# Optimization experiments

Measured on AMD Instinct MI355X. Metric: run time of the kernel, lower is better.

The kernel has to match this reference:

```python
import jax, jax.numpy as jnp
import numpy as np

B, S, D = 4, 2048, 1024


def setup_inputs() -> dict:
    key = jax.random.key(0)
    k1, k2, k3, k4 = jax.random.split(key, 4)
    scale = 1.0 / np.sqrt(D)
    return {
        "X_emb": jax.random.normal(k1, (B, S, D), dtype=jnp.float32),
        "W_q": jax.random.normal(k2, (D, D), dtype=jnp.float32) * scale,
        "W_k": jax.random.normal(k3, (D, D), dtype=jnp.float32) * scale,
        "W_v": jax.random.normal(k4, (D, D), dtype=jnp.float32) * scale,
    }


def reference(X_emb, W_q, W_k, W_v):
    # nn.Linear(bias=False): x @ W.T
    Xq = jnp.einsum('bsd,ed->bse', X_emb, W_q)
    Xk = jnp.einsum('bsd,ed->bse', X_emb, W_k)
    Xv = jnp.einsum('bsd,ed->bse', X_emb, W_v)
    S_len = X_emb.shape[-2]
    # scores [B, S, S]; causal mask (strict upper triangle -> -inf)
    att = jnp.einsum('bqe,bke->bqk', Xq, Xk)
    causal = jnp.tril(jnp.ones((S_len, S_len), dtype=bool))
    att = jnp.where(causal, att, -jnp.inf)
    # note: original masks before scaling; -inf / sqrt(d) is still -inf
    att = att / jnp.sqrt(jnp.asarray(Xk.shape[-1], att.dtype))
    w = jax.nn.softmax(att, axis=-1)
    return jnp.einsum('bqk,bke->bqe', w, Xv)
```

## Files before the change

### kernel.cpp

```cpp
#include <hip/hip_runtime.h>
#include <stdint.h>
#include <math.h>

typedef __attribute__((ext_vector_type(8))) __bf16 bf16x8;
typedef __attribute__((ext_vector_type(4))) float f32x4;

__device__ __forceinline__ unsigned short f2bf(float f) {
    unsigned u = __float_as_uint(f);
    u += 0x7FFF + ((u >> 16) & 1);
    return (unsigned short)(u >> 16);
}
__device__ __forceinline__ float bf2f(unsigned short u) {
    return __uint_as_float((unsigned)u << 16);
}

__global__ __launch_bounds__(256)
void convt_k(const float* __restrict__ X, const float* __restrict__ Wq,
             const float* __restrict__ Wk, const float* __restrict__ Wv,
             unsigned short* __restrict__ Xb, unsigned short* __restrict__ XbT,
             unsigned short* __restrict__ WqT, unsigned short* __restrict__ WkT,
             unsigned short* __restrict__ Wvb) {
    const int S = 2048, D = 1024;
    const int z = blockIdx.z;
    const float* src;
    unsigned short* dstP = nullptr;
    unsigned short* dstT = nullptr;
    int rows;
    if (z < 4)      { src = X + (size_t)z * S * D; dstP = Xb + (size_t)z * S * D;
                      dstT = XbT + (size_t)z * D * S; rows = S; }
    else if (z == 4){ src = Wq; dstT = WqT; rows = D; }
    else if (z == 5){ src = Wk; dstT = WkT; rows = D; }
    else            { src = Wv; dstP = Wvb; rows = D; }
    const int r0 = blockIdx.y * 64, c0 = blockIdx.x * 64;
    if (r0 >= rows) return;

    __shared__ float tile[64][65];
    const int t = threadIdx.x;
    const int tr = t >> 4;
    const int tc4 = t & 15;
#pragma unroll
    for (int p = 0; p < 4; ++p) {
        int r = p * 16 + tr;
        float4 v = *reinterpret_cast<const float4*>(&src[(size_t)(r0 + r) * 1024 + c0 + tc4 * 4]);
        if (dstP) {
            ushort4 o; o.x = f2bf(v.x); o.y = f2bf(v.y); o.z = f2bf(v.z); o.w = f2bf(v.w);
            *reinterpret_cast<ushort4*>(&dstP[(size_t)(r0 + r) * 1024 + c0 + tc4 * 4]) = o;
        }
        if (dstT) {
            tile[r][tc4 * 4 + 0] = v.x; tile[r][tc4 * 4 + 1] = v.y;
            tile[r][tc4 * 4 + 2] = v.z; tile[r][tc4 * 4 + 3] = v.w;
        }
    }
    if (!dstT) return;
    __syncthreads();
    const int ldT = rows;
#pragma unroll
    for (int p = 0; p < 4; ++p) {
        int c = p * 16 + tr;
        ushort4 o;
        o.x = f2bf(tile[tc4 * 4 + 0][c]);
        o.y = f2bf(tile[tc4 * 4 + 1][c]);
        o.z = f2bf(tile[tc4 * 4 + 2][c]);
        o.w = f2bf(tile[tc4 * 4 + 3][c]);
        *reinterpret_cast<ushort4*>(&dstT[(size_t)(c0 + c) * ldT + r0 + tc4 * 4]) = o;
    }
}

__global__ __launch_bounds__(256)
void reduce4_k(const float* __restrict__ p, unsigned short* __restrict__ o, int n4) {
    const int slab = 1024 * 1024 / 4;
    int i = blockIdx.x * blockDim.x + threadIdx.x;
    int stride = gridDim.x * blockDim.x;
    for (; i < n4; i += stride) {
        float4 a = reinterpret_cast<const float4*>(p)[i];
        float4 b = reinterpret_cast<const float4*>(p)[i + slab];
        float4 c = reinterpret_cast<const float4*>(p)[i + 2 * slab];
        float4 d = reinterpret_cast<const float4*>(p)[i + 3 * slab];
        ushort4 u;
        u.x = f2bf(a.x + b.x + c.x + d.x);
        u.y = f2bf(a.y + b.y + c.y + d.y);
        u.z = f2bf(a.z + b.z + c.z + d.z);
        u.w = f2bf(a.w + b.w + c.w + d.w);
        reinterpret_cast<ushort4*>(o)[i] = u;
    }
}

__device__ __forceinline__ void gload16(const unsigned short* g, unsigned short* l) {
    __builtin_amdgcn_global_load_lds(
        (const __attribute__((address_space(1))) unsigned int*)g,
        (__attribute__((address_space(3))) unsigned int*)l, 16, 0, 0);
}

template <typename CT, int MODE>
__global__ __launch_bounds__(256, 2)
void gemm8(const unsigned short* __restrict__ A, const unsigned short* __restrict__ B,
           CT* __restrict__ C, int lda, int ldb, int ldc, int K,
           long long sA, long long sB, long long sC, float scale, int totj)
{
    constexpr int BM = 128, BN = 128;
    constexpr int FM = 4, FN = 4;

    const int nbx = gridDim.x;
    const int nwg = nbx * gridDim.y;
    const int orig = blockIdx.y * nbx + blockIdx.x;
    const int q8 = nwg >> 3, r8 = nwg & 7;
    const int xcd = orig & 7, idx = orig >> 3;
    const int work = (xcd < r8 ? xcd * (q8 + 1) : r8 * (q8 + 1) + (xcd - r8) * q8) + idx;

    A += (long long)blockIdx.z * sA;
    B += (long long)blockIdx.z * sB;
    C += (long long)blockIdx.z * sC;

    __shared__ unsigned short As[2][BM * 64];
    __shared__ unsigned short Bs[2][BN * 64];

    const int t    = threadIdx.x;
    const int lane = t & 63;
    const int wid  = t >> 6;
    const int wm   = wid >> 1, wn = wid & 1;
    const int rsel = lane & 15;
    const int gsel = lane >> 4;
    const int srow = t >> 3;
    const int swz  = ((t & 7) ^ (srow & 7)) * 8;

    auto run_tile = [&](int br, int bc, int kmax, bool first) {
        const int m0 = br * BM, n0 = bc * BN;
        f32x4 acc[FM][FN];
#pragma unroll
        for (int m = 0; m < FM; ++m)
#pragma unroll
            for (int n = 0; n < FN; ++n) acc[m][n] = (f32x4){0.f, 0.f, 0.f, 0.f};

        const unsigned short* gpA[4];
        const unsigned short* gpB[4];
#pragma unroll
        for (int i = 0; i < 4; ++i) {
            gpA[i] = A + (long long)(m0 + srow + 32 * i) * lda + swz;
            gpB[i] = B + (long long)(n0 + srow + 32 * i) * ldb + swz;
        }

        auto stage = [&](int buf) {
#pragma unroll
            for (int i = 0; i < 4; ++i)
                gload16(gpA[i], &As[buf][i * 2048 + t * 8]);
#pragma unroll
            for (int i = 0; i < 4; ++i)
                gload16(gpB[i], &Bs[buf][i * 2048 + t * 8]);
#pragma unroll
            for (int i = 0; i < 4; ++i) { gpA[i] += 64; gpB[i] += 64; }
        };

        const int nk = kmax >> 6;
        if (!first) {
            __builtin_amdgcn_s_barrier();
            __builtin_amdgcn_sched_barrier(0);
        }
        stage(0);

        for (int kt = 0; kt < nk; ++kt) {
            const int c = kt & 1;
            __builtin_amdgcn_s_barrier();
            __builtin_amdgcn_sched_barrier(0);
            if (kt + 1 < nk) {
                stage(c ^ 1);
                asm volatile("s_waitcnt vmcnt(8)" ::: "memory");
            } else {
                asm volatile("s_waitcnt vmcnt(0)" ::: "memory");
            }
            __builtin_amdgcn_s_barrier();
            __builtin_amdgcn_sched_barrier(0);

            bf16x8 aF[FM][2], bF[FN][2];
#pragma unroll
            for (int m = 0; m < FM; ++m)
#pragma unroll
                for (int ks = 0; ks < 2; ++ks) {
                    int r  = wm * (FM * 16) + m * 16 + rsel;
                    int cc = ks * 4 + gsel;
                    aF[m][ks] = *reinterpret_cast<const bf16x8*>(
                        &As[c][r * 64 + ((cc ^ (r & 7)) * 8)]);
                }
#pragma unroll
            for (int n = 0; n < FN; ++n)
#pragma unroll
                for (int ks = 0; ks < 2; ++ks) {
                    int rb = wn * (FN * 16) + n * 16 + rsel;
                    int cc = ks * 4 + gsel;
                    bF[n][ks] = *reinterpret_cast<const bf16x8*>(
                        &Bs[c][rb * 64 + ((cc ^ (rb & 7)) * 8)]);
                }

            __builtin_amdgcn_s_setprio(1);
#pragma unroll
            for (int m = 0; m < FM; ++m)
#pragma unroll
                for (int n = 0; n < FN; ++n)
#pragma unroll
                    for (int ks = 0; ks < 2; ++ks)
                        acc[m][n] = __builtin_amdgcn_mfma_f32_16x16x32_bf16(
                            aF[m][ks], bF[n][ks], acc[m][n], 0, 0, 0);
            __builtin_amdgcn_s_setprio(0);
        }

        const int rowl = gsel * 4;
#pragma unroll
        for (int m = 0; m < FM; ++m) {
#pragma unroll
            for (int n = 0; n < FN; ++n) {
#pragma unroll
                for (int i = 0; i < 4; ++i) {
                    int r  = m0 + wm * (FM * 16) + m * 16 + rowl + i;
                    int cI = n0 + wn * (FN * 16) + n * 16 + rsel;
                    float v = acc[m][n][i] * scale;
                    if constexpr (sizeof(CT) == 2)
                        ((unsigned short*)C)[(long long)r * ldc + cI] = f2bf(v);
                    else
                        ((float*)C)[(long long)r * ldc + cI] = v;
                }
            }
        }
    };

    auto tri = [&](int w, int& br, int& bc) {
        int rr = (int)((sqrtf(8.0f * (float)w + 1.0f) - 1.0f) * 0.5f);
        while ((rr + 1) * (rr + 2) / 2 <= w) ++rr;
        while (rr * (rr + 1) / 2 > w) --rr;
        br = rr; bc = w - rr * (rr + 1) / 2;
    };

    if constexpr (MODE == 0) {
        run_tile(work / nbx, work % nbx, K, true);
    } else if constexpr (MODE == 1) {
        int br, bc;
        tri(work, br, bc);
        run_tile(br, bc, K, true);
        const int e = work >> 4;
        if ((work & 15) == 8 && nwg + e < totj) {
            tri(nwg + e, br, bc);
            run_tile(br, bc, K, false);
        }
    } else {
        const int chunk = work >> 4;
        const int lo    = work & 15;
        const int col   = work & 7;
        const int row   = (lo < 8) ? chunk : 15 - chunk;
        run_tile(row, col, (row + 1) * BM, true);
    }
}

__device__ __forceinline__ float waveMax(float v) {
#pragma unroll
    for (int o = 32; o > 0; o >>= 1) v = fmaxf(v, __shfl_xor(v, o, 64));
    return v;
}
__device__ __forceinline__ float waveSum(float v) {
#pragma unroll
    for (int o = 32; o > 0; o >>= 1) v += __shfl_xor(v, o, 64);
    return v;
}

__global__ __launch_bounds__(256)
void softmax_causal(const unsigned short* __restrict__ S, unsigned short* __restrict__ P,
                    int Slen) {
    __shared__ float e[2048];
    __shared__ float red[4];
    long long row = blockIdx.x;
    int q = (int)(row % Slen);
    const unsigned short* srow = S + row * (long long)Slen;
    unsigned short* prow = P + row * (long long)Slen;
    int len = q + 1;
    int t = threadIdx.x;

    int n8 = len >> 3;
    float mx = -3.0e38f;
    for (int i = t; i < n8; i += 256) {
        uint4 v = reinterpret_cast<const uint4*>(srow)[i];
        float f0 = __uint_as_float(v.x << 16), f1 = __uint_as_float(v.x & 0xffff0000u);
        float f2 = __uint_as_float(v.y << 16), f3 = __uint_as_float(v.y & 0xffff0000u);
        float f4 = __uint_as_float(v.z << 16), f5 = __uint_as_float(v.z & 0xffff0000u);
        float f6 = __uint_as_float(v.w << 16), f7 = __uint_as_float(v.w & 0xffff0000u);
        e[8 * i + 0] = f0; e[8 * i + 1] = f1; e[8 * i + 2] = f2; e[8 * i + 3] = f3;
        e[8 * i + 4] = f4; e[8 * i + 5] = f5; e[8 * i + 6] = f6; e[8 * i + 7] = f7;
        mx = fmaxf(mx, fmaxf(fmaxf(fmaxf(f0, f1), fmaxf(f2, f3)),
                             fmaxf(fmaxf(f4, f5), fmaxf(f6, f7))));
    }
    if (t < (len & 7)) {
        float v = bf2f(srow[n8 * 8 + t]);
        e[n8 * 8 + t] = v;
        mx = fmaxf(mx, v);
    }
    mx = waveMax(mx);
    if ((t & 63) == 0) red[t >> 6] = mx;
    __syncthreads();
    mx = fmaxf(fmaxf(red[0], red[1]), fmaxf(red[2], red[3]));

    float sum = 0.f;
    for (int k = t; k < len; k += 256) {
        float v = __expf(e[k] - mx);
        e[k] = v;
        sum += v;
    }
    sum = waveSum(sum);
    __syncthreads();
    if ((t & 63) == 0) red[t >> 6] = sum;
    __syncthreads();
    sum = red[0] + red[1] + red[2] + red[3];
    float inv = 1.0f / sum;

    int wlim = ((q >> 7) + 1) << 7;
    __syncthreads();
    for (int i = t; i < (wlim >> 2); i += 256) {
        int k = 4 * i;
        ushort4 o;
        o.x = (k + 0 < len) ? f2bf(e[k + 0] * inv) : (unsigned short)0;
        o.y = (k + 1 < len) ? f2bf(e[k + 1] * inv) : (unsigned short)0;
        o.z = (k + 2 < len) ? f2bf(e[k + 2] * inv) : (unsigned short)0;
        o.w = (k + 3 < len) ? f2bf(e[k + 3] * inv) : (unsigned short)0;
        reinterpret_cast<ushort4*>(prow)[i] = o;
    }
}

extern "C" void kernel_launch(void* const* d_in, const int* in_sizes, int n_in,
                              void* d_out, int out_size, void* d_ws, size_t ws_size,
                              hipStream_t stream) {
    const int B = 4, S = 2048, D = 1024;
    const float* X  = (const float*)d_in[0];
    const float* Wq = (const float*)d_in[1];
    const float* Wk = (const float*)d_in[2];
    const float* Wv = (const float*)d_in[3];
    float* out = (float*)d_out;

    char* ws = (char*)d_ws;
    unsigned short* Xb    = (unsigned short*)ws; ws += (size_t)B * S * D * 2;
    unsigned short* XbT   = (unsigned short*)ws; ws += (size_t)B * D * S * 2;
    unsigned short* WqT   = (unsigned short*)ws; ws += (size_t)D * D * 2;
    unsigned short* WkT   = (unsigned short*)ws; ws += (size_t)D * D * 2;
    unsigned short* Wvb   = (unsigned short*)ws; ws += (size_t)D * D * 2;
    unsigned short* MTb   = (unsigned short*)ws; ws += (size_t)D * D * 2;
    unsigned short* XMb   = (unsigned short*)ws; ws += (size_t)B * S * D * 2;
    unsigned short* PXb   = (unsigned short*)ws; ws += (size_t)B * S * D * 2;
    unsigned short* Sc    = (unsigned short*)ws; ws += (size_t)B * S * S * 2;
    unsigned short* P     = (unsigned short*)ws; ws += (size_t)B * S * S * 2;
    float*          Mpart = (float*)ws;          ws += (size_t)4 * D * D * 4;

    convt_k<<<dim3(16, 32, 7), 256, 0, stream>>>(X, Wq, Wk, Wv, Xb, XbT, WqT, WkT, Wvb);

    dim3 blk(256);
    gemm8<float, 0><<<dim3(8, 8, 4), blk, 0, stream>>>(
        WkT, WqT, Mpart, D, D, D, 256, 256, 256, (long long)D * D, 1.0f, 0);
    reduce4_k<<<1024, 256, 0, stream>>>(Mpart, MTb, D * D / 4);

    gemm8<unsigned short, 0><<<dim3(8, 64, 1), blk, 0, stream>>>(
        Xb, MTb, XMb, D, D, D, D, 0, 0, 0, 1.0f, 0);

    gemm8<unsigned short, 1><<<dim3(8, 16, B), blk, 0, stream>>>(
        XMb, Xb, Sc, D, D, S, D, (long long)S * D, (long long)S * D, (long long)S * S,
        0.03125f, 136);

    softmax_causal<<<B * S, 256, 0, stream>>>(Sc, P, S);

    gemm8<unsigned short, 3><<<dim3(8, 16, B), blk, 0, stream>>>(
        P, XbT, PXb, S, S, D, S, (long long)S * S, (long long)D * S, (long long)S * D,
        1.0f, 0);

    gemm8<float, 0><<<dim3(8, 64, 1), blk, 0, stream>>>(
        PXb, Wvb, out, D, D, D, D, 0, 0, 0, 1.0f, 0);
}
```

Before: 169.5 us.

## Precompute V^T via Wv GEMM merged with scores, split-K atomic PV output

The order of the value projection changes: V^T = Wv·X^T is computed per batch inside a merged launch alongside the causal score tiles. P·V^T then writes the final output directly, which removes the separate PX GEMM, the X transpose and one kernel launch. Lower row-blocks of PV are split along K into two halves that accumulate with float atomics into an output zeroed by the conversion kernel. This adds atomic traffic, nondeterministic summation order, and a zeroing pass over the output.

```diff
diff --git a/kernel.cpp b/kernel.cpp
--- a/kernel.cpp
+++ b/kernel.cpp
@@ -17,17 +17,26 @@
 __global__ __launch_bounds__(256)
 void convt_k(const float* __restrict__ X, const float* __restrict__ Wq,
              const float* __restrict__ Wk, const float* __restrict__ Wv,
-             unsigned short* __restrict__ Xb, unsigned short* __restrict__ XbT,
-             unsigned short* __restrict__ WqT, unsigned short* __restrict__ WkT,
-             unsigned short* __restrict__ Wvb) {
+             unsigned short* __restrict__ Xb, unsigned short* __restrict__ WqT,
+             unsigned short* __restrict__ WkT, unsigned short* __restrict__ Wvb,
+             float* __restrict__ outz) {
     const int S = 2048, D = 1024;
     const int z = blockIdx.z;
+    const int t = threadIdx.x;
+    if (z == 7) {
+        const int n4 = 4 * S * D / 4 * 4 / 4;
+        int gid = (blockIdx.y * 16 + blockIdx.x) * 256 + t;
+        int stride = 512 * 256;
+        float4 zz = (float4){0.f, 0.f, 0.f, 0.f};
+        for (int i = gid; i < 4 * S * D / 4; i += stride)
+            reinterpret_cast<float4*>(outz)[i] = zz;
+        return;
+    }
     const float* src;
     unsigned short* dstP = nullptr;
     unsigned short* dstT = nullptr;
     int rows;
-    if (z < 4)      { src = X + (size_t)z * S * D; dstP = Xb + (size_t)z * S * D;
-                      dstT = XbT + (size_t)z * D * S; rows = S; }
+    if (z < 4)      { src = X + (size_t)z * S * D; dstP = Xb + (size_t)z * S * D; rows = S; }
     else if (z == 4){ src = Wq; dstT = WqT; rows = D; }
     else if (z == 5){ src = Wk; dstT = WkT; rows = D; }
     else            { src = Wv; dstP = Wvb; rows = D; }
@@ -35,7 +44,6 @@
     if (r0 >= rows) return;
 
     __shared__ float tile[64][65];
-    const int t = threadIdx.x;
     const int tr = t >> 4;
     const int tc4 = t & 15;
 #pragma unroll
@@ -53,7 +61,6 @@
     }
     if (!dstT) return;
     __syncthreads();
-    const int ldT = rows;
 #pragma unroll
     for (int p = 0; p < 4; ++p) {
         int c = p * 16 + tr;
@@ -62,7 +69,7 @@
         o.y = f2bf(tile[tc4 * 4 + 1][c]);
         o.z = f2bf(tile[tc4 * 4 + 2][c]);
         o.w = f2bf(tile[tc4 * 4 + 3][c]);
-        *reinterpret_cast<ushort4*>(&dstT[(size_t)(c0 + c) * ldT + r0 + tc4 * 4]) = o;
+        *reinterpret_cast<ushort4*>(&dstT[(size_t)(c0 + c) * 1024 + r0 + tc4 * 4]) = o;
     }
 }
 
@@ -91,29 +98,13 @@
         (__attribute__((address_space(3))) unsigned int*)l, 16, 0, 0);
 }
 
-template <typename CT, int MODE>
-__global__ __launch_bounds__(256, 2)
-void gemm8(const unsigned short* __restrict__ A, const unsigned short* __restrict__ B,
-           CT* __restrict__ C, int lda, int ldb, int ldc, int K,
-           long long sA, long long sB, long long sC, float scale, int totj)
+template <typename CT, bool ATOMIC>
+__device__ __forceinline__ void core_tile(
+    const unsigned short* __restrict__ A, const unsigned short* __restrict__ B,
+    CT* __restrict__ C, int lda, int ldb, int ldc,
+    int m0, int n0, int kst, int nk, float scale, bool first,
+    unsigned short* AsB, unsigned short* BsB)
 {
-    constexpr int BM = 128, BN = 128;
-    constexpr int FM = 4, FN = 4;
-
-    const int nbx = gridDim.x;
-    const int nwg = nbx * gridDim.y;
-    const int orig = blockIdx.y * nbx + blockIdx.x;
-    const int q8 = nwg >> 3, r8 = nwg & 7;
-    const int xcd = orig & 7, idx = orig >> 3;
-    const int work = (xcd < r8 ? xcd * (q8 + 1) : r8 * (q8 + 1) + (xcd - r8) * q8) + idx;
-
-    A += (long long)blockIdx.z * sA;
-    B += (long long)blockIdx.z * sB;
-    C += (long long)blockIdx.z * sC;
-
-    __shared__ unsigned short As[2][BM * 64];
-    __shared__ unsigned short Bs[2][BN * 64];
-
     const int t    = threadIdx.x;
     const int lane = t & 63;
     const int wid  = t >> 6;
@@ -123,128 +114,194 @@
     const int srow = t >> 3;
     const int swz  = ((t & 7) ^ (srow & 7)) * 8;
 
-    auto run_tile = [&](int br, int bc, int kmax, bool first) {
-        const int m0 = br * BM, n0 = bc * BN;
-        f32x4 acc[FM][FN];
-#pragma unroll
-        for (int m = 0; m < FM; ++m)
-#pragma unroll
-            for (int n = 0; n < FN; ++n) acc[m][n] = (f32x4){0.f, 0.f, 0.f, 0.f};
-
-        const unsigned short* gpA[4];
-        const unsigned short* gpB[4];
-#pragma unroll
-        for (int i = 0; i < 4; ++i) {
-            gpA[i] = A + (long long)(m0 + srow + 32 * i) * lda + swz;
-            gpB[i] = B + (long long)(n0 + srow + 32 * i) * ldb + swz;
+    f32x4 acc[4][4];
+#pragma unroll
+    for (int m = 0; m < 4; ++m)
+#pragma unroll
+        for (int n = 0; n < 4; ++n) acc[m][n] = (f32x4){0.f, 0.f, 0.f, 0.f};
+
+    const unsigned short* gpA[4];
+    const unsigned short* gpB[4];
+#pragma unroll
+    for (int i = 0; i < 4; ++i) {
+        gpA[i] = A + (long long)(m0 + srow + 32 * i) * lda + kst * 64 + swz;
+        gpB[i] = B + (long long)(n0 + srow + 32 * i) * ldb + kst * 64 + swz;
+    }
+
+    auto stage = [&](int buf) {
+#pragma unroll
+        for (int i = 0; i < 4; ++i)
+            gload16(gpA[i], &AsB[buf * 8192 + i * 2048 + t * 8]);
+#pragma unroll
+        for (int i = 0; i < 4; ++i)
+            gload16(gpB[i], &BsB[buf * 8192 + i * 2048 + t * 8]);
+#pragma unroll
+        for (int i = 0; i < 4; ++i) { gpA[i] += 64; gpB[i] += 64; }
+    };
+
+    if (!first) {
+        __builtin_amdgcn_s_barrier();
+        __builtin_amdgcn_sched_barrier(0);
+    }
+    stage(0);
+
+    for (int kt = 0; kt < nk; ++kt) {
+        const int c = kt & 1;
+        __builtin_amdgcn_s_barrier();
+        __builtin_amdgcn_sched_barrier(0);
+        if (kt + 1 < nk) {
+            stage(c ^ 1);
+            asm volatile("s_waitcnt vmcnt(8)" ::: "memory");
+        } else {
+            asm volatile("s_waitcnt vmcnt(0)" ::: "memory");
         }
-
-        auto stage = [&](int buf) {
-#pragma unroll
-            for (int i = 0; i < 4; ++i)
-                gload16(gpA[i], &As[buf][i * 2048 + t * 8]);
-#pragma unroll
-            for (int i = 0; i < 4; ++i)
-                gload16(gpB[i], &Bs[buf][i * 2048 + t * 8]);
-#pragma unroll
-            for (int i = 0; i < 4; ++i) { gpA[i] += 64; gpB[i] += 64; }
-        };
-
-        const int nk = kmax >> 6;
-        if (!first) {
-            __builtin_amdgcn_s_barrier();
-            __builtin_amdgcn_sched_barrier(0);
+        __builtin_amdgcn_s_barrier();
+        __builtin_amdgcn_sched_barrier(0);
+
+        bf16x8 aF[4][2], bF[4][2];
+#pragma unroll
+        for (int m = 0; m < 4; ++m)
+#pragma unroll
+            for (int ks = 0; ks < 2; ++ks) {
+                int r  = wm * 64 + m * 16 + rsel;
+                int cc = ks * 4 + gsel;
+                aF[m][ks] = *reinterpret_cast<const bf16x8*>(
+                    &AsB[c * 8192 + r * 64 + ((cc ^ (r & 7)) * 8)]);
+            }
+#pragma unroll
+        for (int n = 0; n < 4; ++n)
+#pragma unroll
+            for (int ks = 0; ks < 2; ++ks) {
+                int rb = wn * 64 + n * 16 + rsel;
+                int cc = ks * 4 + gsel;
+                bF[n][ks] = *reinterpret_cast<const bf16x8*>(
+                    &BsB[c * 8192 + rb * 64 + ((cc ^ (rb & 7)) * 8)]);
+            }
+
+        __builtin_amdgcn_s_setprio(1);
+#pragma unroll
+        for (int m = 0; m < 4; ++m)
+#pragma unroll
+            for (int n = 0; n < 4; ++n)
+#pragma unroll
+                for (int ks = 0; ks < 2; ++ks)
+                    acc[m][n] = __builtin_amdgcn_mfma_f32_16x16x32_bf16(
+                        aF[m][ks], bF[n][ks], acc[m][n], 0, 0, 0);
+        __builtin_amdgcn_s_setprio(0);
+    }
+
+    const int rowl = gsel * 4;
+#pragma unroll
+    for (int m = 0; m < 4; ++m)
+#pragma unroll
+        for (int n = 0; n < 4; ++n)
+#pragma unroll
+            for (int i = 0; i < 4; ++i) {
+                int r  = m0 + wm * 64 + m * 16 + rowl + i;
+                int cI = n0 + wn * 64 + n * 16 + rsel;
+                float v = acc[m][n][i] * scale;
+                if constexpr (sizeof(CT) == 2)
+                    ((unsigned short*)C)[(long long)r * ldc + cI] = f2bf(v);
+                else if constexpr (ATOMIC)
+                    unsafeAtomicAdd((float*)&C[(long long)r * ldc + cI], v);
+                else
+                    ((float*)C)[(long long)r * ldc + cI] = v;
+            }
+}
+
+__device__ __forceinline__ void tri_decode(int w, int& br, int& bc) {
+    int rr = (int)((sqrtf(8.0f * (float)w + 1.0f) - 1.0f) * 0.5f);
+    while ((rr + 1) * (rr + 2) / 2 <= w) ++rr;
+    while (rr * (rr + 1) / 2 > w) --rr;
+    br = rr; bc = w - rr * (rr + 1) / 2;
+}
+
+template <typename CT>
+__global__ __launch_bounds__(256, 2)
+void gemm0(const unsigned short* __restrict__ A, const unsigned short* __restrict__ B,
+           CT* __restrict__ C, int lda, int ldb, int ldc, int K,
+           long long sA, long long sB, long long sC, float scale)
+{
+    __shared__ unsigned short As[2 * 8192];
+    __shared__ unsigned short Bs[2 * 8192];
+    const int nbx = gridDim.x;
+    const int nwg = nbx * gridDim.y;
+    const int orig = blockIdx.y * nbx + blockIdx.x;
+    const int q8 = nwg >> 3, r8 = nwg & 7;
+    const int xcd = orig & 7, idx = orig >> 3;
+    const int work = (xcd < r8 ? xcd * (q8 + 1) : r8 * (q8 + 1) + (xcd - r8) * q8) + idx;
+    core_tile<CT, false>(A + (long long)blockIdx.z * sA, B + (long long)blockIdx.z * sB,
+                         C + (long long)blockIdx.z * sC, lda, ldb, ldc,
+                         (work / nbx) * 128, (work % nbx) * 128, 0, K >> 6, scale, true,
+                         As, Bs);
+}
+
+__global__ __launch_bounds__(256, 2)
+void gemm_mrg(const unsigned short* __restrict__ XM, const unsigned short* __restrict__ Xb,
+              unsigned short* __restrict__ Sc, const unsigned short* __restrict__ Wv,
+              unsigned short* __restrict__ Vt)
+{
+    const int S = 2048, D = 1024;
+    const long long SD = (long long)S * D, SS = (long long)S * S, DS = (long long)D * S;
+    __shared__ unsigned short As[2 * 8192];
+    __shared__ unsigned short Bs[2 * 8192];
+    const int orig = blockIdx.x;
+    const int work = (orig & 7) * 128 + (orig >> 3);
+    const int xcdc = work >> 7, idx = work & 127;
+
+    if (idx < 4) {
+        int d = xcdc * 4 + idx;
+        int b = d >> 3, dp = d & 7;
+        const unsigned short* A = XM + b * SD;
+        const unsigned short* B = Xb + b * SD;
+        unsigned short* C = Sc + b * SS;
+        core_tile<unsigned short, false>(A, B, C, D, D, S,
+            (2 * dp) * 128, (2 * dp) * 128, 0, 16, 0.03125f, true, As, Bs);
+        core_tile<unsigned short, false>(A, B, C, D, D, S,
+            (2 * dp + 1) * 128, (2 * dp + 1) * 128, 0, 16, 0.03125f, false, As, Bs);
+    } else {
+        int j = xcdc * 124 + (idx - 4);
+        if (j < 480) {
+            int b = j / 120, tt = j % 120;
+            int rr, cc;
+            tri_decode(tt, rr, cc);
+            int br = rr + 1, bc = tt - rr * (rr + 1) / 2;
+            core_tile<unsigned short, false>(XM + b * SD, Xb + b * SD, Sc + b * SS,
+                D, D, S, br * 128, bc * 128, 0, 16, 0.03125f, true, As, Bs);
+        } else {
+            int v = j - 480;
+            int b = v >> 7, u = v & 127;
+            int r = u >> 4, c = u & 15;
+            core_tile<unsigned short, false>(Wv, Xb + b * SD, Vt + b * DS,
+                D, D, S, r * 128, c * 128, 0, 16, 1.0f, true, As, Bs);
         }
-        stage(0);
-
-        for (int kt = 0; kt < nk; ++kt) {
-            const int c = kt & 1;
-            __builtin_amdgcn_s_barrier();
-            __builtin_amdgcn_sched_barrier(0);
-            if (kt + 1 < nk) {
-                stage(c ^ 1);
-                asm volatile("s_waitcnt vmcnt(8)" ::: "memory");
-            } else {
-                asm volatile("s_waitcnt vmcnt(0)" ::: "memory");
-            }
-            __builtin_amdgcn_s_barrier();
-            __builtin_amdgcn_sched_barrier(0);
-
-            bf16x8 aF[FM][2], bF[FN][2];
-#pragma unroll
-            for (int m = 0; m < FM; ++m)
-#pragma unroll
-                for (int ks = 0; ks < 2; ++ks) {
-                    int r  = wm * (FM * 16) + m * 16 + rsel;
-                    int cc = ks * 4 + gsel;
-                    aF[m][ks] = *reinterpret_cast<const bf16x8*>(
-                        &As[c][r * 64 + ((cc ^ (r & 7)) * 8)]);
-                }
-#pragma unroll
-            for (int n = 0; n < FN; ++n)
-#pragma unroll
-                for (int ks = 0; ks < 2; ++ks) {
-                    int rb = wn * (FN * 16) + n * 16 + rsel;
-                    int cc = ks * 4 + gsel;
-                    bF[n][ks] = *reinterpret_cast<const bf16x8*>(
-                        &Bs[c][rb * 64 + ((cc ^ (rb & 7)) * 8)]);
-                }
-
-            __builtin_amdgcn_s_setprio(1);
-#pragma unroll
-            for (int m = 0; m < FM; ++m)
-#pragma unroll
-                for (int n = 0; n < FN; ++n)
-#pragma unroll
-                    for (int ks = 0; ks < 2; ++ks)
-                        acc[m][n] = __builtin_amdgcn_mfma_f32_16x16x32_bf16(
-                            aF[m][ks], bF[n][ks], acc[m][n], 0, 0, 0);
-            __builtin_amdgcn_s_setprio(0);
-        }
-
-        const int rowl = gsel * 4;
-#pragma unroll
-        for (int m = 0; m < FM; ++m) {
-#pragma unroll
-            for (int n = 0; n < FN; ++n) {
-#pragma unroll
-                for (int i = 0; i < 4; ++i) {
-                    int r  = m0 + wm * (FM * 16) + m * 16 + rowl + i;
-                    int cI = n0 + wn * (FN * 16) + n * 16 + rsel;
-                    float v = acc[m][n][i] * scale;
-                    if constexpr (sizeof(CT) == 2)
-                        ((unsigned short*)C)[(long long)r * ldc + cI] = f2bf(v);
-                    else
-                        ((float*)C)[(long long)r * ldc + cI] = v;
-                }
-            }
-        }
-    };
-
-    auto tri = [&](int w, int& br, int& bc) {
-        int rr = (int)((sqrtf(8.0f * (float)w + 1.0f) - 1.0f) * 0.5f);
-        while ((rr + 1) * (rr + 2) / 2 <= w) ++rr;
-        while (rr * (rr + 1) / 2 > w) --rr;
-        br = rr; bc = w - rr * (rr + 1) / 2;
-    };
-
-    if constexpr (MODE == 0) {
-        run_tile(work / nbx, work % nbx, K, true);
-    } else if constexpr (MODE == 1) {
-        int br, bc;
-        tri(work, br, bc);
-        run_tile(br, bc, K, true);
-        const int e = work >> 4;
-        if ((work & 15) == 8 && nwg + e < totj) {
-            tri(nwg + e, br, bc);
-            run_tile(br, bc, K, false);
-        }
+    }
+}
+
+__global__ __launch_bounds__(256, 2)
+void gemm_pv(const unsigned short* __restrict__ P, const unsigned short* __restrict__ Vt,
+             float* __restrict__ out)
+{
+    const int S = 2048, D = 1024;
+    const long long SS = (long long)S * S, DS = (long long)D * S, SD = (long long)S * D;
+    __shared__ unsigned short As[2 * 8192];
+    __shared__ unsigned short Bs[2 * 8192];
+    const int orig = blockIdx.x;
+    const int work = (orig & 7) * 96 + (orig >> 3);
+    if (work < 512) {
+        int b = work >> 7, u = work & 127;
+        int r = 8 + (u >> 4);
+        int rest = u & 15;
+        int c = rest >> 1, h = rest & 1;
+        int nk = r + 1;
+        core_tile<float, true>(P + b * SS, Vt + b * DS, out + b * SD,
+            S, S, D, r * 128, c * 128, h * nk, nk, 1.0f, true, As, Bs);
     } else {
-        const int chunk = work >> 4;
-        const int lo    = work & 15;
-        const int col   = work & 7;
-        const int row   = (lo < 8) ? chunk : 15 - chunk;
-        run_tile(row, col, (row + 1) * BM, true);
+        int a = work - 512;
+        int b = a >> 6, u = a & 63;
+        int r = u >> 3, c = u & 7;
+        core_tile<float, false>(P + b * SS, Vt + b * DS, out + b * SD,
+            S, S, D, r * 128, c * 128, 0, 2 * (r + 1), 1.0f, true, As, Bs);
     }
 }
 
@@ -332,37 +389,29 @@
 
     char* ws = (char*)d_ws;
     unsigned short* Xb    = (unsigned short*)ws; ws += (size_t)B * S * D * 2;
-    unsigned short* XbT   = (unsigned short*)ws; ws += (size_t)B * D * S * 2;
     unsigned short* WqT   = (unsigned short*)ws; ws += (size_t)D * D * 2;
     unsigned short* WkT   = (unsigned short*)ws; ws += (size_t)D * D * 2;
     unsigned short* Wvb   = (unsigned short*)ws; ws += (size_t)D * D * 2;
     unsigned short* MTb   = (unsigned short*)ws; ws += (size_t)D * D * 2;
     unsigned short* XMb   = (unsigned short*)ws; ws += (size_t)B * S * D * 2;
-    unsigned short* PXb   = (unsigned short*)ws; ws += (size_t)B * S * D * 2;
+    unsigned short* Vt    = (unsigned short*)ws; ws += (size_t)B * D * S * 2;
     unsigned short* Sc    = (unsigned short*)ws; ws += (size_t)B * S * S * 2;
     unsigned short* P     = (unsigned short*)ws; ws += (size_t)B * S * S * 2;
     float*          Mpart = (float*)ws;          ws += (size_t)4 * D * D * 4;
 
-    convt_k<<<dim3(16, 32, 7), 256, 0, stream>>>(X, Wq, Wk, Wv, Xb, XbT, WqT, WkT, Wvb);
+    convt_k<<<dim3(16, 32, 8), 256, 0, stream>>>(X, Wq, Wk, Wv, Xb, WqT, WkT, Wvb, out);
 
     dim3 blk(256);
-    gemm8<float, 0><<<dim3(8, 8, 4), blk, 0, stream>>>(
-        WkT, WqT, Mpart, D, D, D, 256, 256, 256, (long long)D * D, 1.0f, 0);
+    gemm0<float><<<dim3(8, 8, 4), blk, 0, stream>>>(
+        WkT, WqT, Mpart, D, D, D, 256, 256, 256, (long long)D * D, 1.0f);
     reduce4_k<<<1024, 256, 0, stream>>>(Mpart, MTb, D * D / 4);
 
-    gemm8<unsigned short, 0><<<dim3(8, 64, 1), blk, 0, stream>>>(
-        Xb, MTb, XMb, D, D, D, D, 0, 0, 0, 1.0f, 0);
-
-    gemm8<unsigned short, 1><<<dim3(8, 16, B), blk, 0, stream>>>(
-        XMb, Xb, Sc, D, D, S, D, (long long)S * D, (long long)S * D, (long long)S * S,
-        0.03125f, 136);
+    gemm0<unsigned short><<<dim3(8, 64, 1), blk, 0, stream>>>(
+        Xb, MTb, XMb, D, D, D, D, 0, 0, 0, 1.0f);
+
+    gemm_mrg<<<dim3(1024, 1, 1), blk, 0, stream>>>(XMb, Xb, Sc, Wvb, Vt);
 
     softmax_causal<<<B * S, 256, 0, stream>>>(Sc, P, S);
 
-    gemm8<unsigned short, 3><<<dim3(8, 16, B), blk, 0, stream>>>(
-        P, XbT, PXb, S, S, D, S, (long long)S * S, (long long)D * S, (long long)S * D,
-        1.0f, 0);
-
-    gemm8<float, 0><<<dim3(8, 64, 1), blk, 0, stream>>>(
-        PXb, Wvb, out, D, D, D, D, 0, 0, 0, 1.0f, 0);
-}
+    gemm_pv<<<dim3(768, 1, 1), blk, 0, stream>>>(P, Vt, out);
+}
```

Measured after the change: 163.3 us. -3.7%, faster.
